# Kernel tuning notes

Measured on AMD Instinct MI355X. Metric: run time of the kernel, lower is better.

## Reference

```python
import jax, jax.numpy as jnp
import numpy as np

B, T, C = 4, 1024, 768
E, K = 8, 2               # n_exp, top_k
N = B * T                 # num_tokens
# eval-mode capacity: floor(K * eval_capacity(2.0) * N / E), rounded even, >= min_capacity(4)
CAP = 2048


def setup_inputs() -> dict:
    key = jax.random.key(0)
    k0, k1, k2, k3 = jax.random.split(key, 4)
    s = 0.02
    return {
        "x": jax.random.normal(k0, (B, T, C), jnp.float32),
        "w_g": jax.random.normal(k1, (E, C), jnp.float32) * s,
        "c_fc": jax.random.normal(k2, (E, C, 4 * C), jnp.float32) * s,
        "fc_bias": jnp.zeros((E, 1, 4 * C), jnp.float32),
        "c_proj": jax.random.normal(k3, (E, 4 * C, C), jnp.float32) * s,
        "proj_bias": jnp.zeros((E, 1, C), jnp.float32),
    }


def reference(x, w_g, c_fc, fc_bias, c_proj, proj_bias):
    xf = x.reshape(N, C)
    # ---- Router ----
    logits = xf @ w_g.T                                        # [N, E]
    top_v, top_i = jax.lax.top_k(logits, K)                    # [N, K]
    rows = jnp.arange(N)[:, None]
    masked = jnp.full((N, E), -jnp.inf, logits.dtype).at[rows, top_i].set(top_v)
    probs = jax.nn.softmax(masked, axis=-1)                    # [N, E] (zero off top-k)
    exp_mask = jax.nn.one_hot(top_i, E, dtype=jnp.float32)     # [N, K, E]
    exp_mask = exp_mask.transpose(1, 0, 2)                     # [K, N, E]
    # position of each assignment within its expert queue (top-1 assignments first)
    rank = jnp.cumsum(exp_mask.reshape(K * N, E), axis=0) - 1.0
    rank = rank.reshape(K, N, E)
    exp_mask = exp_mask * (rank < CAP)                         # drop over-capacity tokens
    rank_id = jnp.sum(exp_mask * rank, axis=-1).astype(jnp.int32)  # [K, N]
    exp_w = exp_mask * probs[None]                             # [K, N, E]
    rank_sc = jax.nn.one_hot(rank_id, CAP, dtype=jnp.float32)  # [K, N, CAP]
    cb_weight = jnp.einsum('kne,knc->nec', exp_w, rank_sc)     # [N, E, CAP] combine weights
    sec_mask = (cb_weight != 0).astype(xf.dtype)               # [N, E, CAP] dispatch mask
    # ---- Dispatch + batched experts (per-expert MLP via bmm) ----
    exp_in = jnp.einsum('nec,nd->ecd', sec_mask, xf)           # [E, CAP, C]
    h = jax.nn.gelu(jnp.einsum('ecd,edf->ecf', exp_in, c_fc) + fc_bias, approximate=False)
    exp_out = jnp.einsum('ecf,efd->ecd', h, c_proj) + proj_bias  # [E, CAP, C]
    # ---- Combine ----
    out = jnp.einsum('nec,ecd->nd', cb_weight, exp_out)        # [N, C]
    return out.reshape(B, T, C)
```

## Files before the change

### kernel.cpp

```cpp
#include <hip/hip_runtime.h>
#include <hip/hip_bf16.h>
#include <math.h>

#define N_TOK 4096
#define CDIM  768
#define E_EXP 8
#define CAPC  2048
#define HDIM  3072

typedef __attribute__((ext_vector_type(8))) short short8;
typedef __attribute__((ext_vector_type(4))) float floatx4;

#define VMCNT(n) asm volatile("s_waitcnt vmcnt(" #n ")" ::: "memory")
#define LGKM(n)  asm volatile("s_waitcnt lgkmcnt(" #n ")" ::: "memory")
#define SB0()    __builtin_amdgcn_sched_barrier(0)

static __device__ __forceinline__ unsigned short f2bf(float f) {
  __hip_bfloat16 h = __float2bfloat16(f);
  return __builtin_bit_cast(unsigned short, h);
}

__global__ __launch_bounds__(256)
void transpose_convert(const float* __restrict__ in, __hip_bfloat16* __restrict__ out,
                       int R, int Cc)
{
  __shared__ float tile[32][33];
  const int e  = blockIdx.z;
  const int c0 = blockIdx.x * 32;
  const int r0 = blockIdx.y * 32;
  const float* ie = in + (size_t)e * R * Cc;
  __hip_bfloat16* oe = out + (size_t)e * Cc * R;
  const int t = threadIdx.x;
  {
    const int r = t >> 3, c = (t & 7) * 4;
    const float4 v = *(const float4*)(ie + (size_t)(r0 + r) * Cc + c0 + c);
    tile[r][c + 0] = v.x; tile[r][c + 1] = v.y; tile[r][c + 2] = v.z; tile[r][c + 3] = v.w;
  }
  __syncthreads();
  {
    const int cc = t >> 3, rr = (t & 7) * 4;
    ushort4 o;
    o.x = f2bf(tile[rr + 0][cc]);
    o.y = f2bf(tile[rr + 1][cc]);
    o.z = f2bf(tile[rr + 2][cc]);
    o.w = f2bf(tile[rr + 3][cc]);
    *(ushort4*)((unsigned short*)oe + (size_t)(c0 + cc) * R + r0 + rr) = o;
  }
}

__global__ __launch_bounds__(256)
void router_kernel(const float* __restrict__ x, const float* __restrict__ wg,
                   int* __restrict__ eidx, float* __restrict__ pval)
{
  const int wv = threadIdx.x >> 6, lane = threadIdx.x & 63;
  const int n = blockIdx.x * 4 + wv;
  const float* xr = x + (size_t)n * CDIM;
  float acc[E_EXP] = {0.f, 0.f, 0.f, 0.f, 0.f, 0.f, 0.f, 0.f};
#pragma unroll
  for (int i = 0; i < CDIM / 64; ++i) {
    const float xv = xr[i * 64 + lane];
#pragma unroll
    for (int e = 0; e < E_EXP; ++e)
      acc[e] = fmaf(xv, wg[e * CDIM + i * 64 + lane], acc[e]);
  }
#pragma unroll
  for (int e = 0; e < E_EXP; ++e) {
#pragma unroll
    for (int off = 32; off > 0; off >>= 1)
      acc[e] += __shfl_xor(acc[e], off);
  }
  if (lane == 0) {
    int e0 = 0; float v0 = acc[0];
#pragma unroll
    for (int e = 1; e < E_EXP; ++e) if (acc[e] > v0) { v0 = acc[e]; e0 = e; }
    int e1 = -1; float v1 = -3.4e38f;
#pragma unroll
    for (int e = 0; e < E_EXP; ++e) if (e != e0 && acc[e] > v1) { v1 = acc[e]; e1 = e; }
    const float ex = __expf(v1 - v0);
    const float inv = 1.f / (1.f + ex);
    eidx[n] = e0; eidx[N_TOK + n] = e1;
    pval[n] = inv; pval[N_TOK + n] = ex * inv;
  }
}

__global__ void init_slots(int* __restrict__ p)
{
  p[blockIdx.x * 256 + threadIdx.x] = -1;
}

__global__ __launch_bounds__(256)
void scan_kernel(const int* __restrict__ eidx, int* __restrict__ slot,
                 int* __restrict__ slot_token, int* __restrict__ ecnt)
{
  const int t = threadIdx.x;
  const int base = t * 32;
  int e_local[32];
  int cnt[E_EXP] = {0, 0, 0, 0, 0, 0, 0, 0};
#pragma unroll
  for (int i = 0; i < 32; ++i) {
    const int e = eidx[base + i];
    e_local[i] = e;
    cnt[e]++;
  }
  __shared__ int hist[256][E_EXP];
#pragma unroll
  for (int e = 0; e < E_EXP; ++e) hist[t][e] = cnt[e];
  __syncthreads();
  for (int off = 1; off < 256; off <<= 1) {
    int v[E_EXP] = {0, 0, 0, 0, 0, 0, 0, 0};
    if (t >= off) {
#pragma unroll
      for (int e = 0; e < E_EXP; ++e) v[e] = hist[t - off][e];
    }
    __syncthreads();
    if (t >= off) {
#pragma unroll
      for (int e = 0; e < E_EXP; ++e) hist[t][e] += v[e];
    }
    __syncthreads();
  }
  if (t == 255) {
#pragma unroll
    for (int e = 0; e < E_EXP; ++e) {
      const int tot = hist[255][e];
      ecnt[e] = tot < CAPC ? tot : CAPC;
    }
  }
  int run[E_EXP];
#pragma unroll
  for (int e = 0; e < E_EXP; ++e) run[e] = hist[t][e] - cnt[e];
#pragma unroll
  for (int i = 0; i < 32; ++i) {
    const int a = base + i;
    const int e = e_local[i];
    const int r = run[e]++;
    const int s = (r < CAPC) ? r : -1;
    slot[a] = s;
    if (s >= 0) slot_token[e * CAPC + s] = (a < N_TOK) ? a : (a - N_TOK);
  }
}

__global__ __launch_bounds__(256)
void dispatch_kernel(const float* __restrict__ x, const int* __restrict__ slot_token,
                     __hip_bfloat16* __restrict__ xin)
{
  const int wv = threadIdx.x >> 6, lane = threadIdx.x & 63;
  const int s = blockIdx.x * 4 + wv;
  const int n = slot_token[s];
  if (n < 0) return;
  unsigned short* orow = (unsigned short*)xin + (size_t)s * CDIM;
  const float4* xr = (const float4*)(x + (size_t)n * CDIM);
#pragma unroll
  for (int i = 0; i < 3; ++i) {
    const float4 v = xr[i * 64 + lane];
    ushort4 o;
    o.x = f2bf(v.x); o.y = f2bf(v.y); o.z = f2bf(v.z); o.w = f2bf(v.w);
    *(ushort4*)(orow + (size_t)(i * 64 + lane) * 4) = o;
  }
}

template<int BN, int Kc>
__device__ __forceinline__ void stageT(const __hip_bfloat16* __restrict__ Ae,
                                       const __hip_bfloat16* __restrict__ Be,
                                       char* dst, int kt, int wv, int lane)
{
  constexpr int NI = BN / 64;
  const int r = wv * 8 + (lane >> 3);
  const int kb = ((lane & 7) * 16) ^ ((r & 7) << 4);
  const char* As = (const char*)Ae + (size_t)kt * 128 + (size_t)r * (Kc * 2) + kb;
  const char* Bs = (const char*)Be + (size_t)kt * 128 + (size_t)r * (Kc * 2) + kb;
#pragma unroll
  for (int j = 0; j < 4; ++j)
    __builtin_amdgcn_global_load_lds(
        (const __attribute__((address_space(1))) unsigned int*)(As + (size_t)j * 64 * Kc * 2),
        (__attribute__((address_space(3))) unsigned int*)(dst + j * 8192 + wv * 1024), 16, 0, 0);
#pragma unroll
  for (int j = 0; j < NI; ++j)
    __builtin_amdgcn_global_load_lds(
        (const __attribute__((address_space(1))) unsigned int*)(Bs + (size_t)j * 64 * Kc * 2),
        (__attribute__((address_space(3))) unsigned int*)(dst + 32768 + j * 8192 + wv * 1024), 16, 0, 0);
}

template<int BN, int Kc, int VME, bool ST, int BUF>
__device__ __forceinline__ void ktileT(int kt, char* lds,
                                       const __hip_bfloat16* __restrict__ Ae,
                                       const __hip_bfloat16* __restrict__ Be,
                                       floatx4 (&acc)[8][BN / 64],
                                       int wm, int wn, int fr, int fk, int wv, int lane)
{
  constexpr int NI = BN / 64;
  constexpr int BUFS = (256 + BN) * 128;
  if constexpr (VME == 8) VMCNT(8);
  else if constexpr (VME == 7) VMCNT(7);
  else VMCNT(0);
  SB0();
  __builtin_amdgcn_s_barrier();
  SB0();
  const char* bufA = lds + BUF * BUFS;
  const char* bufB = bufA + 32768;
  short8 a[4][2], b[NI][2];

#pragma unroll
  for (int mi = 0; mi < 4; ++mi) {
    const int lr = wm * 128 + mi * 16 + fr;
#pragma unroll
    for (int kk = 0; kk < 2; ++kk)
      a[mi][kk] = *(const short8*)(bufA + lr * 128 + ((kk * 64 + fk * 16) ^ ((lr & 7) << 4)));
  }
#pragma unroll
  for (int ni = 0; ni < 2; ++ni) {
    const int lj = wn * (BN / 4) + ni * 16 + fr;
#pragma unroll
    for (int kk = 0; kk < 2; ++kk)
      b[ni][kk] = *(const short8*)(bufB + lj * 128 + ((kk * 64 + fk * 16) ^ ((lj & 7) << 4)));
  }
  __builtin_amdgcn_s_setprio(1);
#pragma unroll
  for (int kk = 0; kk < 2; ++kk)
#pragma unroll
    for (int mi = 0; mi < 4; ++mi)
#pragma unroll
      for (int ni = 0; ni < 2; ++ni)
        acc[mi][ni] = __builtin_amdgcn_mfma_f32_16x16x32_bf16(a[mi][kk], b[ni][kk], acc[mi][ni], 0, 0, 0);
  __builtin_amdgcn_s_setprio(0);
  SB0();

#pragma unroll
  for (int ni = 2; ni < NI; ++ni) {
    const int lj = wn * (BN / 4) + ni * 16 + fr;
#pragma unroll
    for (int kk = 0; kk < 2; ++kk)
      b[ni][kk] = *(const short8*)(bufB + lj * 128 + ((kk * 64 + fk * 16) ^ ((lj & 7) << 4)));
  }
  __builtin_amdgcn_s_setprio(1);
#pragma unroll
  for (int kk = 0; kk < 2; ++kk)
#pragma unroll
    for (int mi = 0; mi < 4; ++mi)
#pragma unroll
      for (int ni = 2; ni < NI; ++ni)
        acc[mi][ni] = __builtin_amdgcn_mfma_f32_16x16x32_bf16(a[mi][kk], b[ni][kk], acc[mi][ni], 0, 0, 0);
  __builtin_amdgcn_s_setprio(0);
  SB0();

#pragma unroll
  for (int mi = 0; mi < 4; ++mi) {
    const int lr = wm * 128 + 64 + mi * 16 + fr;
#pragma unroll
    for (int kk = 0; kk < 2; ++kk)
      a[mi][kk] = *(const short8*)(bufA + lr * 128 + ((kk * 64 + fk * 16) ^ ((lr & 7) << 4)));
  }
  __builtin_amdgcn_s_setprio(1);
#pragma unroll
  for (int kk = 0; kk < 2; ++kk)
#pragma unroll
    for (int mi = 0; mi < 4; ++mi)
#pragma unroll
      for (int ni = 0; ni < 2; ++ni)
        acc[4 + mi][ni] = __builtin_amdgcn_mfma_f32_16x16x32_bf16(a[mi][kk], b[ni][kk], acc[4 + mi][ni], 0, 0, 0);
  __builtin_amdgcn_s_setprio(0);
  SB0();
  __builtin_amdgcn_s_barrier();
  SB0();
  if constexpr (ST)
    stageT<BN, Kc>(Ae, Be, lds + BUF * BUFS, kt + 2, wv, lane);
  SB0();

  __builtin_amdgcn_s_setprio(1);
#pragma unroll
  for (int kk = 0; kk < 2; ++kk)
#pragma unroll
    for (int mi = 0; mi < 4; ++mi)
#pragma unroll
      for (int ni = 2; ni < NI; ++ni)
        acc[4 + mi][ni] = __builtin_amdgcn_mfma_f32_16x16x32_bf16(a[mi][kk], b[ni][kk], acc[4 + mi][ni], 0, 0, 0);
  __builtin_amdgcn_s_setprio(0);
  SB0();
}

template<int GELU_OUT, int BN, int Kc, int NBX>
__global__ __launch_bounds__(512, 2)
void gemmT(const __hip_bfloat16* __restrict__ A, const __hip_bfloat16* __restrict__ Bt,
           const float* __restrict__ bias, void* __restrict__ Cout,
           const int* __restrict__ ecnt)
{
  constexpr int NI  = BN / 64;
  constexpr int L   = 4 + NI;
  constexpr int Nc  = NBX * BN;
  constexpr int ntk = Kc / 64;
  constexpr int BUFS = (256 + BN) * 128;
  extern __shared__ __align__(16) char lds[];

  const int nwg = gridDim.x;
  int wg = blockIdx.x;
  wg = (wg & 7) * (nwg >> 3) + (wg >> 3);
  const int e = wg / (NBX * 8);
  const int rem = wg % (NBX * 8);
  const int by = rem / NBX, bx = rem % NBX;
  if (by * 256 >= ecnt[e]) return;
  const int t = threadIdx.x, wv = t >> 6, lane = t & 63;
  const int wm = wv >> 2, wn = wv & 3;
  const int fr = lane & 15, fk = lane >> 4;

  const __hip_bfloat16* Ae = A + (size_t)e * CAPC * Kc + (size_t)by * 256 * Kc;
  const __hip_bfloat16* Be = Bt + (size_t)e * Nc * Kc + (size_t)bx * BN * Kc;

  floatx4 acc[8][NI] = {};

  stageT<BN, Kc>(Ae, Be, lds, 0, wv, lane);
  stageT<BN, Kc>(Ae, Be, lds + BUFS, 1, wv, lane);
  SB0();

#pragma unroll 1
  for (int kt = 0; kt < ntk - 2; kt += 2) {
    ktileT<BN, Kc, L, true, 0>(kt, lds, Ae, Be, acc, wm, wn, fr, fk, wv, lane);
    ktileT<BN, Kc, L, true, 1>(kt + 1, lds, Ae, Be, acc, wm, wn, fr, fk, wv, lane);
  }
  ktileT<BN, Kc, L, false, 0>(ntk - 2, lds, Ae, Be, acc, wm, wn, fr, fk, wv, lane);
  ktileT<BN, Kc, 0, false, 1>(ntk - 1, lds, Ae, Be, acc, wm, wn, fr, fk, wv, lane);

  const float* be = bias + (size_t)e * Nc;
  const size_t cbase = (size_t)e * CAPC * Nc;
  const int m0 = by * 256, n0 = bx * BN;

  if constexpr (GELU_OUT) {
    unsigned short* ep = (unsigned short*)(lds + wv * 2048);
    unsigned short* Cb = (unsigned short*)Cout + cbase;
    float bcol[NI];
#pragma unroll
    for (int ni = 0; ni < NI; ++ni) bcol[ni] = be[n0 + wn * (BN / 4) + ni * 16 + fr];
#pragma unroll
    for (int mi = 0; mi < 8; ++mi) {
#pragma unroll
      for (int ni = 0; ni < NI; ++ni)
#pragma unroll
        for (int j = 0; j < 4; ++j) {
          float v = acc[mi][ni][j] + bcol[ni];
          v = 0.5f * v * (1.0f + erff(v * 0.70710678118654752f));
          const int row = fk * 4 + j;
          *(unsigned short*)((char*)ep + row * 128 + ((ni * 32 + fr * 2) ^ (fk << 5))) = f2bf(v);
        }
      LGKM(0); SB0();
      const int r = lane & 15;
      const int grow = m0 + wm * 128 + mi * 16 + r;
#pragma unroll
      for (int it = 0; it < 2; ++it) {
        const int q = (lane >> 4) + it * 4;
        const short8 vv = *(const short8*)((char*)ep + r * 128 + ((q * 16) ^ ((r >> 2) << 5)));
        *(short8*)(Cb + (size_t)grow * Nc + n0 + wn * 64 + q * 8) = vv;
      }
      LGKM(0); SB0();
    }
  } else {
#pragma unroll
    for (int ni = 0; ni < NI; ++ni) {
      const int col = n0 + wn * (BN / 4) + ni * 16 + fr;
      const float b = be[col];
#pragma unroll
      for (int mi = 0; mi < 8; ++mi) {
        const int rbase = m0 + wm * 128 + mi * 16 + fk * 4;
#pragma unroll
        for (int j = 0; j < 4; ++j) {
          ((float*)Cout)[cbase + (size_t)(rbase + j) * Nc + col] = acc[mi][ni][j] + b;
        }
      }
    }
  }
}

__device__ __forceinline__ void stage_ab(const __hip_bfloat16* Ae, const __hip_bfloat16* Be,
                                         char* lds, int K, int kt, int isB,
                                         int wv, int lane)
{
  const char* src = (const char*)(isB ? Be : Ae);
  char* dst = lds + (kt & 1) * 32768 + isB * 16384;
#pragma unroll
  for (int j = 0; j < 4; ++j) {
    const int li = j * 32 + wv * 8 + (lane >> 3);
    const int kb = ((lane & 7) * 16) ^ ((li & 7) << 4);
    const char* g = src + ((size_t)li * K + (size_t)kt * 64) * 2 + kb;
    char* lp = dst + j * 4096 + wv * 1024;
    __builtin_amdgcn_global_load_lds((const __attribute__((address_space(1))) unsigned int*)g,
                                     (__attribute__((address_space(3))) unsigned int*)lp, 16, 0, 0);
  }
}

template<int VME, bool S2>
__device__ __forceinline__ void ktile2(int kt, char* lds,
                                       const __hip_bfloat16* Ae, const __hip_bfloat16* Be,
                                       int K, floatx4 (&acc)[4][4],
                                       int wm, int wn, int fr, int fk, int wv, int lane)
{
  if constexpr (VME == 8) VMCNT(8); else VMCNT(0);
  __builtin_amdgcn_s_barrier();
  SB0();
  const char* bufA = lds + ((kt & 1) ? 32768 : 0);
  const char* bufB = bufA + 16384;
  short8 a[4][2], b[4][2];
#pragma unroll
  for (int mi = 0; mi < 4; ++mi) {
    const int lr = wm * 64 + mi * 16 + fr;
    a[mi][0] = *(const short8*)(bufA + lr * 128 + ((fk * 16) ^ ((lr & 7) << 4)));
  }
#pragma unroll
  for (int ni = 0; ni < 4; ++ni) {
    const int lj = wn * 64 + ni * 16 + fr;
    b[ni][0] = *(const short8*)(bufB + lj * 128 + ((fk * 16) ^ ((lj & 7) << 4)));
  }
  SB0();
#pragma unroll
  for (int mi = 0; mi < 4; ++mi) {
    const int lr = wm * 64 + mi * 16 + fr;
    a[mi][1] = *(const short8*)(bufA + lr * 128 + ((64 + fk * 16) ^ ((lr & 7) << 4)));
  }
#pragma unroll
  for (int ni = 0; ni < 4; ++ni) {
    const int lj = wn * 64 + ni * 16 + fr;
    b[ni][1] = *(const short8*)(bufB + lj * 128 + ((64 + fk * 16) ^ ((lj & 7) << 4)));
  }
  SB0();
  LGKM(8); SB0();
  __builtin_amdgcn_s_setprio(1);
#pragma unroll
  for (int mi = 0; mi < 4; ++mi)
#pragma unroll
    for (int ni = 0; ni < 4; ++ni)
      acc[mi][ni] = __builtin_amdgcn_mfma_f32_16x16x32_bf16(a[mi][0], b[ni][0], acc[mi][ni], 0, 0, 0);
  __builtin_amdgcn_s_setprio(0);
  SB0();
  LGKM(0); SB0();
  __builtin_amdgcn_s_setprio(1);
#pragma unroll
  for (int mi = 0; mi < 4; ++mi)
#pragma unroll
    for (int ni = 0; ni < 4; ++ni)
      acc[mi][ni] = __builtin_amdgcn_mfma_f32_16x16x32_bf16(a[mi][1], b[ni][1], acc[mi][ni], 0, 0, 0);
  __builtin_amdgcn_s_setprio(0);
  SB0();
  __builtin_amdgcn_s_barrier();
  if (S2) {
    stage_ab(Ae, Be, lds, K, kt + 2, 0, wv, lane);
    stage_ab(Ae, Be, lds, K, kt + 2, 1, wv, lane);
  }
  SB0();
}

__global__ __launch_bounds__(256, 2)
void gemm2b(const __hip_bfloat16* __restrict__ A, const __hip_bfloat16* __restrict__ Bt,
            const float* __restrict__ bias, float* __restrict__ Cout,
            int M, int Nn, int K, int nbx, int nby, const int* __restrict__ ecnt)
{
  extern __shared__ __align__(16) char lds[];
  const int nwg = gridDim.x;
  int wg = blockIdx.x;
  wg = (wg & 7) * (nwg >> 3) + (wg >> 3);
  const int e = wg / (nbx * nby);
  const int rem = wg % (nbx * nby);
  const int by = rem / nbx, bx = rem % nbx;
  if (by * 128 >= ecnt[e]) return;
  const int t = threadIdx.x, wv = t >> 6, lane = t & 63;
  const int wm = wv >> 1, wn = wv & 1;
  const int fr = lane & 15, fk = lane >> 4;
  const int ntk = K >> 6;

  const __hip_bfloat16* Ae = A + (size_t)e * M * K + (size_t)by * 128 * K;
  const __hip_bfloat16* Be = Bt + (size_t)e * Nn * K + (size_t)bx * 128 * K;

  floatx4 acc[4][4] = {};

  stage_ab(Ae, Be, lds, K, 0, 0, wv, lane);
  stage_ab(Ae, Be, lds, K, 0, 1, wv, lane);
  stage_ab(Ae, Be, lds, K, 1, 0, wv, lane);
  stage_ab(Ae, Be, lds, K, 1, 1, wv, lane);
  SB0();

  for (int kt = 0; kt < ntk - 2; ++kt)
    ktile2<8, true>(kt, lds, Ae, Be, K, acc, wm, wn, fr, fk, wv, lane);
  ktile2<8, false>(ntk - 2, lds, Ae, Be, K, acc, wm, wn, fr, fk, wv, lane);
  ktile2<0, false>(ntk - 1, lds, Ae, Be, K, acc, wm, wn, fr, fk, wv, lane);

  const float* be = bias + (size_t)e * Nn;
  const size_t cbase = (size_t)e * M * Nn;
  const int m0 = by * 128, n0 = bx * 128;
#pragma unroll
  for (int ni = 0; ni < 4; ++ni) {
    const int col = n0 + wn * 64 + ni * 16 + fr;
    const float b = be[col];
#pragma unroll
    for (int mi = 0; mi < 4; ++mi) {
      const int rbase = m0 + wm * 64 + mi * 16 + fk * 4;
#pragma unroll
      for (int j = 0; j < 4; ++j) {
        Cout[cbase + (size_t)(rbase + j) * Nn + col] = acc[mi][ni][j] + b;
      }
    }
  }
}

__global__ __launch_bounds__(256)
void combine_kernel(const float* __restrict__ eout, const int* __restrict__ eidx,
                    const float* __restrict__ pval, const int* __restrict__ slot,
                    float* __restrict__ out)
{
  const int wv = threadIdx.x >> 6, lane = threadIdx.x & 63;
  const int n = blockIdx.x * 4 + wv;
  const int e0 = eidx[n], e1 = eidx[N_TOK + n];
  int s0 = slot[n], s1 = slot[N_TOK + n];
  const float w0 = (s0 >= 0) ? pval[n] : 0.f;
  const float w1 = (s1 >= 0) ? pval[N_TOK + n] : 0.f;
  s0 = (s0 >= 0) ? s0 : 0;
  s1 = (s1 >= 0) ? s1 : 0;
  const float4* r0 = (const float4*)(eout + ((size_t)e0 * CAPC + s0) * CDIM);
  const float4* r1 = (const float4*)(eout + ((size_t)e1 * CAPC + s1) * CDIM);
  float4* o = (float4*)(out + (size_t)n * CDIM);
#pragma unroll
  for (int i = 0; i < 3; ++i) {
    const float4 a = r0[i * 64 + lane];
    const float4 b = r1[i * 64 + lane];
    float4 c;
    c.x = w0 * a.x + w1 * b.x;
    c.y = w0 * a.y + w1 * b.y;
    c.z = w0 * a.z + w1 * b.z;
    c.w = w0 * a.w + w1 * b.w;
    o[i * 64 + lane] = c;
  }
}

extern "C" void kernel_launch(void* const* d_in, const int* in_sizes, int n_in,
                              void* d_out, int out_size, void* d_ws, size_t ws_size,
                              hipStream_t stream)
{
  const float* x   = (const float*)d_in[0];
  const float* wg  = (const float*)d_in[1];
  const float* cfc = (const float*)d_in[2];
  const float* fcb = (const float*)d_in[3];
  const float* cpr = (const float*)d_in[4];
  const float* prb = (const float*)d_in[5];
  float* out = (float*)d_out;

  char* ws = (char*)d_ws;
  size_t off = 0;
  auto take = [&](size_t bytes) -> void* {
    void* p = ws + off;
    off += (bytes + 255) & ~(size_t)255;
    return p;
  };
  __hip_bfloat16* wfcT = (__hip_bfloat16*)take((size_t)E_EXP * HDIM * CDIM * 2);
  __hip_bfloat16* wprT = (__hip_bfloat16*)take((size_t)E_EXP * CDIM * HDIM * 2);
  __hip_bfloat16* xin  = (__hip_bfloat16*)take((size_t)E_EXP * CAPC * CDIM * 2);
  __hip_bfloat16* hbuf = (__hip_bfloat16*)take((size_t)E_EXP * CAPC * HDIM * 2);
  float*          eout = (float*)take((size_t)E_EXP * CAPC * CDIM * 4);
  int*   eidx = (int*)take((size_t)2 * N_TOK * 4);
  float* pv   = (float*)take((size_t)2 * N_TOK * 4);
  int*   slot = (int*)take((size_t)2 * N_TOK * 4);
  int*   stok = (int*)take((size_t)E_EXP * CAPC * 4);
  int*   ecnt = (int*)take((size_t)E_EXP * 4);

  hipFuncSetAttribute((const void*)gemmT<1, 256, CDIM, 12>,
                      hipFuncAttributeMaxDynamicSharedMemorySize, 131072);
  hipFuncSetAttribute((const void*)gemm2b,
                      hipFuncAttributeMaxDynamicSharedMemorySize, 65536);

  transpose_convert<<<dim3(HDIM / 32, CDIM / 32, E_EXP), 256, 0, stream>>>(cfc, wfcT, CDIM, HDIM);
  transpose_convert<<<dim3(CDIM / 32, HDIM / 32, E_EXP), 256, 0, stream>>>(cpr, wprT, HDIM, CDIM);

  router_kernel<<<N_TOK / 4, 256, 0, stream>>>(x, wg, eidx, pv);
  init_slots<<<(E_EXP * CAPC) / 256, 256, 0, stream>>>(stok);
  scan_kernel<<<1, 256, 0, stream>>>(eidx, slot, stok, ecnt);
  dispatch_kernel<<<(E_EXP * CAPC) / 4, 256, 0, stream>>>(x, stok, xin);

  gemmT<1, 256, CDIM, 12><<<768, 512, 131072, stream>>>(xin, wfcT, fcb, hbuf, ecnt);
  gemm2b<<<768, 256, 65536, stream>>>(hbuf, wprT, prb, eout, CAPC, CDIM, HDIM, 6, 16, ecnt);

  combine_kernel<<<N_TOK / 4, 256, 0, stream>>>(eout, eidx, pv, slot, out);
}
```

Before: 204.5 us.

## Build compact per-expert work lists so GEMM blocks map only to populated tiles

The scan kernel now writes compact lists of (expert, row-tile) pairs for both expert GEMMs, sized from each expert's actual token count. The GEMM kernels index these lists instead of a fixed grid, spreading the active tiles evenly across the 8-way XCD interleave rather than leaving empty tiles that exit early. This aims to balance load across compute units and cut wasted block launches. The cost is a serial list build by one thread in the scan kernel and an extra indirection load at the start of each GEMM block.

```diff
diff --git a/kernel.cpp b/kernel.cpp
--- a/kernel.cpp
+++ b/kernel.cpp
@@ -90,7 +90,9 @@
 
 __global__ __launch_bounds__(256)
 void scan_kernel(const int* __restrict__ eidx, int* __restrict__ slot,
-                 int* __restrict__ slot_token, int* __restrict__ ecnt)
+                 int* __restrict__ slot_token, int* __restrict__ ecnt,
+                 int* __restrict__ work1, int* __restrict__ work2,
+                 int* __restrict__ wcnt)
 {
   const int t = threadIdx.x;
   const int base = t * 32;
@@ -103,6 +105,7 @@
     cnt[e]++;
   }
   __shared__ int hist[256][E_EXP];
+  __shared__ int secnt[E_EXP];
 #pragma unroll
   for (int e = 0; e < E_EXP; ++e) hist[t][e] = cnt[e];
   __syncthreads();
@@ -123,8 +126,23 @@
 #pragma unroll
     for (int e = 0; e < E_EXP; ++e) {
       const int tot = hist[255][e];
-      ecnt[e] = tot < CAPC ? tot : CAPC;
+      const int c = tot < CAPC ? tot : CAPC;
+      ecnt[e] = c;
+      secnt[e] = c;
     }
+  }
+  __syncthreads();
+  if (t == 0) {
+    int n1 = 0, n2 = 0;
+    for (int e = 0; e < E_EXP; ++e) {
+      const int c = secnt[e];
+      const int t1 = (c + 255) >> 8;
+      for (int b = 0; b < t1; ++b) work1[n1++] = (e << 8) | b;
+      const int t2 = (c + 127) >> 7;
+      for (int b = 0; b < t2; ++b) work2[n2++] = (e << 8) | b;
+    }
+    wcnt[0] = n1 * 12;
+    wcnt[1] = n2 * 6;
   }
   int run[E_EXP];
 #pragma unroll
@@ -282,7 +300,7 @@
 __global__ __launch_bounds__(512, 2)
 void gemmT(const __hip_bfloat16* __restrict__ A, const __hip_bfloat16* __restrict__ Bt,
            const float* __restrict__ bias, void* __restrict__ Cout,
-           const int* __restrict__ ecnt)
+           const int* __restrict__ work, const int* __restrict__ wcnt)
 {
   constexpr int NI  = BN / 64;
   constexpr int L   = 4 + NI;
@@ -291,13 +309,16 @@
   constexpr int BUFS = (256 + BN) * 128;
   extern __shared__ __align__(16) char lds[];
 
-  const int nwg = gridDim.x;
-  int wg = blockIdx.x;
-  wg = (wg & 7) * (nwg >> 3) + (wg >> 3);
-  const int e = wg / (NBX * 8);
-  const int rem = wg % (NBX * 8);
-  const int by = rem / NBX, bx = rem % NBX;
-  if (by * 256 >= ecnt[e]) return;
+  const int T = wcnt[0];
+  const int bId = blockIdx.x;
+  const int cpx = (T + 7) >> 3;
+  if ((bId >> 3) >= cpx) return;
+  const int idx = (bId & 7) * cpx + (bId >> 3);
+  if (idx >= T) return;
+  const int p = idx / NBX, bx = idx % NBX;
+  const int w = work[p];
+  const int e = w >> 8, by = w & 255;
+
   const int t = threadIdx.x, wv = t >> 6, lane = t & 63;
   const int wm = wv >> 2, wn = wv & 3;
   const int fr = lane & 15, fk = lane >> 4;
@@ -448,16 +469,20 @@
 __global__ __launch_bounds__(256, 2)
 void gemm2b(const __hip_bfloat16* __restrict__ A, const __hip_bfloat16* __restrict__ Bt,
             const float* __restrict__ bias, float* __restrict__ Cout,
-            int M, int Nn, int K, int nbx, int nby, const int* __restrict__ ecnt)
+            int M, int Nn, int K,
+            const int* __restrict__ work, const int* __restrict__ wcnt)
 {
   extern __shared__ __align__(16) char lds[];
-  const int nwg = gridDim.x;
-  int wg = blockIdx.x;
-  wg = (wg & 7) * (nwg >> 3) + (wg >> 3);
-  const int e = wg / (nbx * nby);
-  const int rem = wg % (nbx * nby);
-  const int by = rem / nbx, bx = rem % nbx;
-  if (by * 128 >= ecnt[e]) return;
+  const int T = wcnt[1];
+  const int bId = blockIdx.x;
+  const int cpx = (T + 7) >> 3;
+  if ((bId >> 3) >= cpx) return;
+  const int idx = (bId & 7) * cpx + (bId >> 3);
+  if (idx >= T) return;
+  const int p = idx / 6, bx = idx % 6;
+  const int w = work[p];
+  const int e = w >> 8, by = w & 255;
+
   const int t = threadIdx.x, wv = t >> 6, lane = t & 63;
   const int wm = wv >> 1, wn = wv & 1;
   const int fr = lane & 15, fk = lane >> 4;
@@ -555,6 +580,9 @@
   int*   slot = (int*)take((size_t)2 * N_TOK * 4);
   int*   stok = (int*)take((size_t)E_EXP * CAPC * 4);
   int*   ecnt = (int*)take((size_t)E_EXP * 4);
+  int*   work1 = (int*)take((size_t)64 * 4);
+  int*   work2 = (int*)take((size_t)128 * 4);
+  int*   wcnt = (int*)take((size_t)2 * 4);
 
   hipFuncSetAttribute((const void*)gemmT<1, 256, CDIM, 12>,
                       hipFuncAttributeMaxDynamicSharedMemorySize, 131072);
@@ -566,11 +594,11 @@
 
   router_kernel<<<N_TOK / 4, 256, 0, stream>>>(x, wg, eidx, pv);
   init_slots<<<(E_EXP * CAPC) / 256, 256, 0, stream>>>(stok);
-  scan_kernel<<<1, 256, 0, stream>>>(eidx, slot, stok, ecnt);
+  scan_kernel<<<1, 256, 0, stream>>>(eidx, slot, stok, ecnt, work1, work2, wcnt);
   dispatch_kernel<<<(E_EXP * CAPC) / 4, 256, 0, stream>>>(x, stok, xin);
 
-  gemmT<1, 256, CDIM, 12><<<768, 512, 131072, stream>>>(xin, wfcT, fcb, hbuf, ecnt);
-  gemm2b<<<768, 256, 65536, stream>>>(hbuf, wprT, prb, eout, CAPC, CDIM, HDIM, 6, 16, ecnt);
+  gemmT<1, 256, CDIM, 12><<<768, 512, 131072, stream>>>(xin, wfcT, fcb, hbuf, work1, wcnt);
+  gemm2b<<<768, 256, 65536, stream>>>(hbuf, wprT, prb, eout, CAPC, CDIM, HDIM, work2, wcnt);
 
   combine_kernel<<<N_TOK / 4, 256, 0, stream>>>(eout, eidx, pv, slot, out);
 }
```

Result: faster. 200.3 us (-2.1%).
